# Optimization experiments

Hardware: AMD Instinct MI355X
Metric: run time of the kernel (lower is better)

## Reference

```python
import jax, jax.numpy as jnp
import numpy as np

B, N, F_IN, F_OUT, E = 2, 20000, 256, 256, 640000


def setup_inputs() -> dict:
    key = jax.random.key(0)
    k1, k2, k3, k4, k5, k6 = jax.random.split(key, 6)
    x = jax.random.normal(k1, (B, N, F_IN), dtype=jnp.float32)
    edge_index = jax.random.randint(k2, (2, E), 0, N, dtype=jnp.int64)
    s = 1.0 / np.sqrt(F_IN)
    W_l = jax.random.normal(k3, (F_OUT, F_IN), dtype=jnp.float32) * s
    b_l = jax.random.normal(k4, (F_OUT,), dtype=jnp.float32) * s
    W_r = jax.random.normal(k5, (F_OUT, F_IN), dtype=jnp.float32) * s
    return {"x": x, "edge_index": edge_index, "W_l": W_l, "b_l": b_l, "W_r": W_r}


def reference(x, edge_index, W_l, b_l, W_r):
    # PyG SAGEConv (mean aggr): out = lin_l(mean_{j in N(i)} x_j) + lin_r(x_i), ReLU on top.
    src = edge_index[0]  # message sources (x_j)
    tgt = edge_index[1]  # aggregation targets (i)
    n = x.shape[1]
    # gather messages: [B,E,F] -> [E,B,F] so segment axis is leading
    msgs = jnp.transpose(x[:, src, :], (1, 0, 2))
    agg = jax.ops.segment_sum(msgs, tgt, num_segments=n)  # [N,B,F]
    deg = jax.ops.segment_sum(jnp.ones((tgt.shape[0],), dtype=x.dtype), tgt, num_segments=n)
    agg = agg / jnp.maximum(deg, 1.0)[:, None, None]
    agg = jnp.transpose(agg, (1, 0, 2))  # [B,N,F]
    out = jnp.einsum('bnf,of->bno', agg, W_l) + b_l + jnp.einsum('bnf,of->bno', x, W_r)
    return jax.nn.relu(out)
```

## Files before the change

### kernel.cpp

```cpp
#include <hip/hip_runtime.h>

#define F 256
#define R 8
#define RCAP 24

typedef short short8 __attribute__((ext_vector_type(8)));
typedef float floatx4 __attribute__((ext_vector_type(4)));
typedef float floatx2 __attribute__((ext_vector_type(2)));
typedef unsigned short u16;
typedef unsigned int u32;

__device__ __forceinline__ u16 f2bf(float f) {
    u32 u = __float_as_uint(f);
    u += 0x7fffu + ((u >> 16) & 1u);
    return (u16)(u >> 16);
}
__device__ __forceinline__ u32 pack2bf(float lo, float hi) {
    return (u32)f2bf(lo) | ((u32)f2bf(hi) << 16);
}

__device__ __forceinline__ void async16(const u16* g, u16* l) {
    __builtin_amdgcn_global_load_lds(
        (const __attribute__((address_space(1))) u32*)g,
        (__attribute__((address_space(3))) u32*)l, 16, 0, 0);
}

__global__ __launch_bounds__(256) void fused_scatter_cast(
    const float* __restrict__ x, u16* __restrict__ xb, u32* __restrict__ xf8,
    int nx4,
    const float* __restrict__ Wl, u16* __restrict__ Wlb,
    const float* __restrict__ Wr, u16* __restrict__ Wrb, int nw4,
    const int* __restrict__ src, const int* __restrict__ tgt,
    u32* __restrict__ counts, u16* __restrict__ sorted, int E)
{
    int b = blockIdx.x;
    const int eblocks = (E + 255) >> 8;
    if (b < eblocks) {
        const int e = b * 256 + threadIdx.x;
        if (e >= E) return;
        const int r = b & (R - 1);
        const int t = tgt[e];
        const int s = src[e];
        const u32 slot = atomicAdd(&counts[t * R + r], 1u);
        if (slot < RCAP)
            sorted[(size_t)t * (R * RCAP) + r * RCAP + slot] = (u16)s;
        return;
    }
    b -= eblocks;
    const int xblocks = nx4 >> 8;
    if (b < xblocks) {
        const int idx = b * 256 + threadIdx.x;
        const float4 v = ((const float4*)x)[idx];
        ushort4 o;
        o.x = f2bf(v.x); o.y = f2bf(v.y); o.z = f2bf(v.z); o.w = f2bf(v.w);
        ((ushort4*)xb)[idx] = o;
        u32 p = __builtin_amdgcn_cvt_pk_fp8_f32(v.x, v.y, 0, false);
        p = __builtin_amdgcn_cvt_pk_fp8_f32(v.z, v.w, p, true);
        xf8[idx] = p;
        return;
    }
    b -= xblocks;
    const int wblocks = nw4 >> 8;
    {
        const float* s = (b < wblocks) ? Wl : Wr;
        u16* dst = (b < wblocks) ? Wlb : Wrb;
        if (b >= wblocks) b -= wblocks;
        const int idx = b * 256 + threadIdx.x;
        const float4 v = ((const float4*)s)[idx];
        ushort4 o;
        o.x = f2bf(v.x); o.y = f2bf(v.y); o.z = f2bf(v.z); o.w = f2bf(v.w);
        ((ushort4*)dst)[idx] = o;
    }
}

__global__ __launch_bounds__(256) void aggregate_kernel(
    const u32* __restrict__ xf8, const u32* __restrict__ counts,
    const u16* __restrict__ sorted, u16* __restrict__ aggb, int N)
{
    const int node = blockIdx.x * 4 + (threadIdx.x >> 6);
    if (node >= N) return;
    const int l = threadIdx.x & 63;
    const int bsel = l >> 5;
    const int l32 = l & 31;
    const u16* nodebase = sorted + (size_t)node * (R * RCAP);

    const u32* base = xf8 + (size_t)bsel * N * 64 + l32 * 2;

    floatx2 a0 = {0, 0}, a1 = {0, 0}, a2 = {0, 0}, a3 = {0, 0};
    int total = 0;
    #pragma unroll
    for (int r = 0; r < R; ++r) {
        const int cg = (int)counts[node * R + r];
        total += cg;
        const int cnt = min(cg, RCAP);
        const u16* run = nodebase + r * RCAP;
        int e = 0;
        for (; e + 4 <= cnt; e += 4) {
            const uint2 u0 = *(const uint2*)(base + (size_t)run[e + 0] * 64);
            const uint2 u1 = *(const uint2*)(base + (size_t)run[e + 1] * 64);
            const uint2 u2 = *(const uint2*)(base + (size_t)run[e + 2] * 64);
            const uint2 u3 = *(const uint2*)(base + (size_t)run[e + 3] * 64);
            a0 += __builtin_amdgcn_cvt_pk_f32_fp8(u0.x, false)
                + __builtin_amdgcn_cvt_pk_f32_fp8(u1.x, false)
                + __builtin_amdgcn_cvt_pk_f32_fp8(u2.x, false)
                + __builtin_amdgcn_cvt_pk_f32_fp8(u3.x, false);
            a1 += __builtin_amdgcn_cvt_pk_f32_fp8(u0.x, true)
                + __builtin_amdgcn_cvt_pk_f32_fp8(u1.x, true)
                + __builtin_amdgcn_cvt_pk_f32_fp8(u2.x, true)
                + __builtin_amdgcn_cvt_pk_f32_fp8(u3.x, true);
            a2 += __builtin_amdgcn_cvt_pk_f32_fp8(u0.y, false)
                + __builtin_amdgcn_cvt_pk_f32_fp8(u1.y, false)
                + __builtin_amdgcn_cvt_pk_f32_fp8(u2.y, false)
                + __builtin_amdgcn_cvt_pk_f32_fp8(u3.y, false);
            a3 += __builtin_amdgcn_cvt_pk_f32_fp8(u0.y, true)
                + __builtin_amdgcn_cvt_pk_f32_fp8(u1.y, true)
                + __builtin_amdgcn_cvt_pk_f32_fp8(u2.y, true)
                + __builtin_amdgcn_cvt_pk_f32_fp8(u3.y, true);
        }
        for (; e < cnt; ++e) {
            const uint2 u0 = *(const uint2*)(base + (size_t)run[e] * 64);
            a0 += __builtin_amdgcn_cvt_pk_f32_fp8(u0.x, false);
            a1 += __builtin_amdgcn_cvt_pk_f32_fp8(u0.x, true);
            a2 += __builtin_amdgcn_cvt_pk_f32_fp8(u0.y, false);
            a3 += __builtin_amdgcn_cvt_pk_f32_fp8(u0.y, true);
        }
    }

    const float inv = 1.0f / fmaxf((float)total, 1.0f);
    uint4 o;
    o.x = pack2bf(a0.x * inv, a0.y * inv);
    o.y = pack2bf(a1.x * inv, a1.y * inv);
    o.z = pack2bf(a2.x * inv, a2.y * inv);
    o.w = pack2bf(a3.x * inv, a3.y * inv);
    *(uint4*)((u32*)(aggb + (size_t)bsel * N * F) + (size_t)node * 128 + l32 * 4) = o;
}

__global__ __launch_bounds__(256) void gemm_mfma(
    const u16* __restrict__ aggb, const u16* __restrict__ xb,
    const u16* __restrict__ Wlb, const u16* __restrict__ Wrb,
    const float* __restrict__ bl, float* __restrict__ out)
{
    __shared__ u16 ldsA[64 * 32];
    __shared__ u16 ldsB[256 * 32];

    const int tid = threadIdx.x;
    const int w = tid >> 6;
    const int l = tid & 63;
    const int m0 = blockIdx.x * 64;

    floatx4 acc[4][4] = {};

    for (int kc = 0; kc < 16; ++kc) {
        const bool first = kc < 8;
        const int k0 = (first ? kc : kc - 8) * 32;
        const u16* A = first ? aggb : xb;
        const u16* B = first ? Wlb : Wrb;

        async16(A + (size_t)(m0 + (tid >> 2)) * F + k0 + (tid & 3) * 8,
                &ldsA[w * 512]);
        #pragma unroll
        for (int j = 0; j < 4; ++j)
            async16(B + (size_t)(j * 64 + (tid >> 2)) * F + k0 + (tid & 3) * 8,
                    &ldsB[j * 2048 + w * 512]);
        __syncthreads();

        const int kr = (l >> 4) * 8;
        short8 af[4], bfr[4];
        #pragma unroll
        for (int i = 0; i < 4; ++i)
            af[i] = *(const short8*)&ldsA[(i * 16 + (l & 15)) * 32 + kr];
        #pragma unroll
        for (int j = 0; j < 4; ++j)
            bfr[j] = *(const short8*)&ldsB[(w * 64 + j * 16 + (l & 15)) * 32 + kr];
        #pragma unroll
        for (int i = 0; i < 4; ++i)
            #pragma unroll
            for (int j = 0; j < 4; ++j)
                acc[i][j] = __builtin_amdgcn_mfma_f32_16x16x32_bf16(
                    af[i], bfr[j], acc[i][j], 0, 0, 0);
        __syncthreads();
    }

    #pragma unroll
    for (int j = 0; j < 4; ++j) {
        const int col = w * 64 + j * 16 + (l & 15);
        const float bias = bl[col];
        #pragma unroll
        for (int i = 0; i < 4; ++i) {
            const int rbase = m0 + i * 16 + (l >> 4) * 4;
            #pragma unroll
            for (int r = 0; r < 4; ++r)
                out[(size_t)(rbase + r) * F + col] = fmaxf(acc[i][j][r] + bias, 0.0f);
        }
    }
}

extern "C" void kernel_launch(void* const* d_in, const int* in_sizes, int n_in,
                              void* d_out, int out_size, void* d_ws, size_t ws_size,
                              hipStream_t stream)
{
    const float* x  = (const float*)d_in[0];
    const int*   ei = (const int*)d_in[1];
    const float* Wl = (const float*)d_in[2];
    const float* bl = (const float*)d_in[3];
    const float* Wr = (const float*)d_in[4];
    float* out = (float*)d_out;

    const int E = in_sizes[1] / 2;
    const int N = in_sizes[0] / (2 * F);
    const int M = 2 * N;

    const int* src = ei;
    const int* tgt = ei + E;

    u32* counts = (u32*)d_ws;
    u16* sorted = (u16*)(counts + (size_t)N * R);
    u16* xb     = sorted + (size_t)N * R * RCAP;
    u16* aggb   = xb + (size_t)M * F;
    u16* Wlb    = aggb + (size_t)M * F;
    u16* Wrb    = Wlb + F * F;
    u32* xf8    = (u32*)d_out;

    hipMemsetAsync(counts, 0, (size_t)N * R * sizeof(u32), stream);

    const int nx4 = M * F / 4;
    const int nw4 = F * F / 4;
    const int eblocks = (E + 255) / 256;
    const int total_blocks = eblocks + nx4 / 256 + 2 * (nw4 / 256);
    fused_scatter_cast<<<total_blocks, 256, 0, stream>>>(
        x, xb, xf8, nx4, Wl, Wlb, Wr, Wrb, nw4, src, tgt, counts, sorted, E);

    aggregate_kernel<<<(N + 3) / 4, 256, 0, stream>>>(xf8, counts, sorted, aggb, N);

    gemm_mfma<<<M / 64, 256, 0, stream>>>(aggb, xb, Wlb, Wrb, bl, out);
}
```

Baseline: 203.0 us.

## Interleave gathers across sub-buckets and transpose count layout to bucket-major

The aggregation kernel now reads all eight per-bucket counts first, then loops over step up to the max count and issues up to eight independent gathers per step, one from each bucket, instead of walking buckets sequentially with 4-way unrolling. This raises memory-level parallelism for nodes whose edges are spread thinly across buckets (about 4 per bucket on average). The counts array is also transposed to bucket-major (r*N+t), so the scatter atomics from one block land in a contiguous region and the aggregate's count reads coalesce across nodes. The cost is predicated per-bucket branches and more live registers.

New measurement: 206.1 us. No clear change (+1.5%).

```diff
diff --git a/kernel.cpp b/kernel.cpp
--- a/kernel.cpp
+++ b/kernel.cpp
@@ -31,7 +31,7 @@
     const float* __restrict__ Wl, u16* __restrict__ Wlb,
     const float* __restrict__ Wr, u16* __restrict__ Wrb, int nw4,
     const int* __restrict__ src, const int* __restrict__ tgt,
-    u32* __restrict__ counts, u16* __restrict__ sorted, int E)
+    u32* __restrict__ counts, u16* __restrict__ sorted, int E, int N)
 {
     int b = blockIdx.x;
     const int eblocks = (E + 255) >> 8;
@@ -41,7 +41,7 @@
         const int r = b & (R - 1);
         const int t = tgt[e];
         const int s = src[e];
-        const u32 slot = atomicAdd(&counts[t * R + r], 1u);
+        const u32 slot = atomicAdd(&counts[r * N + t], 1u);
         if (slot < RCAP)
             sorted[(size_t)t * (R * RCAP) + r * RCAP + slot] = (u16)s;
         return;
@@ -86,44 +86,34 @@
 
     const u32* base = xf8 + (size_t)bsel * N * 64 + l32 * 2;
 
-    floatx2 a0 = {0, 0}, a1 = {0, 0}, a2 = {0, 0}, a3 = {0, 0};
+    int cs[R];
     int total = 0;
     #pragma unroll
     for (int r = 0; r < R; ++r) {
-        const int cg = (int)counts[node * R + r];
-        total += cg;
-        const int cnt = min(cg, RCAP);
-        const u16* run = nodebase + r * RCAP;
-        int e = 0;
-        for (; e + 4 <= cnt; e += 4) {
-            const uint2 u0 = *(const uint2*)(base + (size_t)run[e + 0] * 64);
-            const uint2 u1 = *(const uint2*)(base + (size_t)run[e + 1] * 64);
-            const uint2 u2 = *(const uint2*)(base + (size_t)run[e + 2] * 64);
-            const uint2 u3 = *(const uint2*)(base + (size_t)run[e + 3] * 64);
-            a0 += __builtin_amdgcn_cvt_pk_f32_fp8(u0.x, false)
-                + __builtin_amdgcn_cvt_pk_f32_fp8(u1.x, false)
-                + __builtin_amdgcn_cvt_pk_f32_fp8(u2.x, false)
-                + __builtin_amdgcn_cvt_pk_f32_fp8(u3.x, false);
-            a1 += __builtin_amdgcn_cvt_pk_f32_fp8(u0.x, true)
-                + __builtin_amdgcn_cvt_pk_f32_fp8(u1.x, true)
-                + __builtin_amdgcn_cvt_pk_f32_fp8(u2.x, true)
-                + __builtin_amdgcn_cvt_pk_f32_fp8(u3.x, true);
-            a2 += __builtin_amdgcn_cvt_pk_f32_fp8(u0.y, false)
-                + __builtin_amdgcn_cvt_pk_f32_fp8(u1.y, false)
-                + __builtin_amdgcn_cvt_pk_f32_fp8(u2.y, false)
-                + __builtin_amdgcn_cvt_pk_f32_fp8(u3.y, false);
-            a3 += __builtin_amdgcn_cvt_pk_f32_fp8(u0.y, true)
-                + __builtin_amdgcn_cvt_pk_f32_fp8(u1.y, true)
-                + __builtin_amdgcn_cvt_pk_f32_fp8(u2.y, true)
-                + __builtin_amdgcn_cvt_pk_f32_fp8(u3.y, true);
-        }
-        for (; e < cnt; ++e) {
-            const uint2 u0 = *(const uint2*)(base + (size_t)run[e] * 64);
-            a0 += __builtin_amdgcn_cvt_pk_f32_fp8(u0.x, false);
-            a1 += __builtin_amdgcn_cvt_pk_f32_fp8(u0.x, true);
-            a2 += __builtin_amdgcn_cvt_pk_f32_fp8(u0.y, false);
-            a3 += __builtin_amdgcn_cvt_pk_f32_fp8(u0.y, true);
-        }
+        const int c = (int)counts[r * N + node];
+        total += c;
+        cs[r] = min(c, RCAP);
+    }
+    int maxc = 0;
+    #pragma unroll
+    for (int r = 0; r < R; ++r) maxc = max(maxc, cs[r]);
+
+    floatx2 a0 = {0, 0}, a1 = {0, 0}, a2 = {0, 0}, a3 = {0, 0};
+    for (int step = 0; step < maxc; ++step) {
+        uint2 u[R];
+        #pragma unroll
+        for (int r = 0; r < R; ++r)
+            if (step < cs[r])
+                u[r] = *(const uint2*)(base +
+                        (size_t)nodebase[r * RCAP + step] * 64);
+        #pragma unroll
+        for (int r = 0; r < R; ++r)
+            if (step < cs[r]) {
+                a0 += __builtin_amdgcn_cvt_pk_f32_fp8(u[r].x, false);
+                a1 += __builtin_amdgcn_cvt_pk_f32_fp8(u[r].x, true);
+                a2 += __builtin_amdgcn_cvt_pk_f32_fp8(u[r].y, false);
+                a3 += __builtin_amdgcn_cvt_pk_f32_fp8(u[r].y, true);
+            }
     }
 
     const float inv = 1.0f / fmaxf((float)total, 1.0f);
@@ -214,21 +204,21 @@
     const int* tgt = ei + E;
 
     u32* counts = (u32*)d_ws;
-    u16* sorted = (u16*)(counts + (size_t)N * R);
+    u16* sorted = (u16*)(counts + (size_t)R * N);
     u16* xb     = sorted + (size_t)N * R * RCAP;
     u16* aggb   = xb + (size_t)M * F;
     u16* Wlb    = aggb + (size_t)M * F;
     u16* Wrb    = Wlb + F * F;
     u32* xf8    = (u32*)d_out;
 
-    hipMemsetAsync(counts, 0, (size_t)N * R * sizeof(u32), stream);
+    hipMemsetAsync(counts, 0, (size_t)R * N * sizeof(u32), stream);
 
     const int nx4 = M * F / 4;
     const int nw4 = F * F / 4;
     const int eblocks = (E + 255) / 256;
     const int total_blocks = eblocks + nx4 / 256 + 2 * (nw4 / 256);
     fused_scatter_cast<<<total_blocks, 256, 0, stream>>>(
-        x, xb, xf8, nx4, Wl, Wlb, Wr, Wrb, nw4, src, tgt, counts, sorted, E);
+        x, xb, xf8, nx4, Wl, Wlb, Wr, Wrb, nw4, src, tgt, counts, sorted, E, N);
 
     aggregate_kernel<<<(N + 3) / 4, 256, 0, stream>>>(xf8, counts, sorted, aggb, N);
 
```
